# Kernel tuning notes

Measured on AMD Instinct MI355X. Metric: run time of the kernel, lower is better.

The kernel has to match this reference:

```python
import jax, jax.numpy as jnp
import numpy as np

B, T, DIM, H, HD = 2, 2048, 1024, 16, 64
ROPE_THETA = 500000.0
EPS = 1e-6
SOFTCAP = 50.0


def _rmsnorm(x, gamma):
    # x: (..., HD)
    rms = jax.lax.rsqrt(jnp.mean(x * x, axis=-1, keepdims=True) + EPS)
    return x * rms * gamma


def _apply_rope(x, cos, sin):
    # x: (B, T, H, HD); cos/sin: (T, HD//2). Pairs are interleaved (even, odd).
    xe = x[..., 0::2]
    xo = x[..., 1::2]
    c = cos[None, :, None, :]
    s = sin[None, :, None, :]
    re = xe * c - xo * s
    im = xe * s + xo * c
    # re-interleave: (..., HD//2, 2) -> (..., HD)
    return jnp.stack([re, im], axis=-1).reshape(x.shape)


def setup_inputs() -> dict:
    key = jax.random.key(0)
    kx, kq, kk, kv, ko = jax.random.split(key, 5)
    x = jax.random.normal(kx, (B, T, DIM), dtype=jnp.float32)
    sc = 0.02
    wq = jax.random.normal(kq, (H * HD, DIM), dtype=jnp.float32) * sc
    wk = jax.random.normal(kk, (HD, DIM), dtype=jnp.float32) * sc
    wv = jax.random.normal(kv, (HD, DIM), dtype=jnp.float32) * sc
    wo = jax.random.normal(ko, (DIM, H * HD), dtype=jnp.float32) * sc
    q_gamma = jnp.ones((HD,), dtype=jnp.float32)
    k_gamma = jnp.ones((HD,), dtype=jnp.float32)
    # RoPE tables (same as torch.polar precompute)
    inv_freq = 1.0 / (ROPE_THETA ** (np.arange(0, HD, 2, dtype=np.float32) / HD))
    t = np.arange(T, dtype=np.float32)
    ang = np.outer(t, inv_freq)  # (T, HD//2)
    freqs_cos = jnp.asarray(np.cos(ang), dtype=jnp.float32)
    freqs_sin = jnp.asarray(np.sin(ang), dtype=jnp.float32)
    # causal additive mask (T, T)
    causal = np.tril(np.ones((T, T), dtype=bool))
    mask = jnp.asarray(np.where(causal, 0.0, -1e9).astype(np.float32))
    return {"x": x, "wq": wq, "wk": wk, "wv": wv, "wo": wo,
            "q_gamma": q_gamma, "k_gamma": k_gamma,
            "freqs_cos": freqs_cos, "freqs_sin": freqs_sin, "mask": mask}


def reference(x, wq, wk, wv, wo, q_gamma, k_gamma, freqs_cos, freqs_sin, mask):
    b, t, _ = x.shape
    q = (x @ wq.T).reshape(b, t, H, HD)            # (B,T,H,HD)
    k = (x @ wk.T).reshape(b, t, 1, HD)            # (B,T,1,HD) single KV head
    v = x @ wv.T                                    # (B,T,HD)
    q = _rmsnorm(q, q_gamma)
    k = _rmsnorm(k, k_gamma)
    q = _apply_rope(q, freqs_cos, freqs_sin)
    k = _apply_rope(k, freqs_cos, freqs_sin)[:, :, 0, :]  # (B,S,HD)
    scale = HD ** -0.5
    # MQA: single K/V head shared across H query heads
    attn = jnp.einsum('bthd,bsd->bhts', q, k) * scale      # (B,H,T,S)
    attn = jnp.tanh(attn / SOFTCAP) * SOFTCAP
    attn = attn + mask[None, None, :, :]
    p = jax.nn.softmax(attn, axis=-1)
    out = jnp.einsum('bhts,bsd->bthd', p, v).reshape(b, t, H * HD)
    return out @ wo.T
```

## Files before the change

kernel.cpp:

```cpp
#include <hip/hip_runtime.h>
#include <hip/hip_bf16.h>
#include <stdint.h>
#include <math.h>

#define B_ 2
#define T_ 2048
#define DIM_ 1024
#define H_ 16
#define HD_ 64
#define NROWS_ (B_*T_)
#define NQKV 1152
#define UNITS_PER_BH 80
#define NUNITS (16 * UNITS_PER_BH)

typedef __bf16 bf16_t;
typedef __attribute__((ext_vector_type(8))) __bf16 bf16x8;
typedef __attribute__((ext_vector_type(4))) __bf16 bf16x4;
typedef __attribute__((ext_vector_type(4))) float f32x4;
typedef __attribute__((ext_vector_type(16))) float f32x16;

__device__ __forceinline__ float wave_sum64(float v) {
#pragma unroll
  for (int off = 32; off > 0; off >>= 1) v += __shfl_xor(v, off, 64);
  return v;
}

__device__ __forceinline__ int cb(int q) {
  int a = q >> 3, r = q & 7;
  return 4 * a * (a + 1) + r * (a + 1);
}

__device__ __forceinline__ bf16_t* swz(bf16_t* base, int row, int col) {
  return (bf16_t*)((char*)base + (row << 7) + (((col << 1) ^ ((row & 7) << 4))));
}

__device__ __forceinline__ f32x16 mfma32(bf16x8 a, bf16x8 b, f32x16 c) {
  return __builtin_amdgcn_mfma_f32_32x32x16_bf16(a, b, c, 0, 0, 0);
}

__device__ __forceinline__ unsigned cvt_pk(float lo, float hi) {
  unsigned r;
  asm("v_cvt_pk_bf16_f32 %0, %1, %2" : "=v"(r) : "v"(lo), "v"(hi));
  return r;
}
__device__ __forceinline__ void plswap(unsigned& x, unsigned& y) {
  asm volatile("v_permlane32_swap_b32 %0, %1" : "+v"(x), "+v"(y));
}

#define C_S0 (NROWS_*DIM_/8)
#define C_S1 (C_S0 + DIM_*DIM_/8)
#define C_S2 (C_S1 + HD_*DIM_/8)
#define C_S3 (C_S2 + HD_*DIM_/8)
#define C_S4 (C_S3 + DIM_*DIM_/8)
__global__ __launch_bounds__(256) void cvt_all(
    const float* __restrict__ x, const float* __restrict__ wq,
    const float* __restrict__ wk, const float* __restrict__ wv,
    const float* __restrict__ wo, bf16_t* __restrict__ xb,
    bf16_t* __restrict__ wqkvb, bf16_t* __restrict__ wob) {
  int i = blockIdx.x * 256 + threadIdx.x;
  if (i >= C_S4) return;
  const float* src; bf16_t* dst; int j;
  if (i < C_S0)      { src = x;  dst = xb; j = i; }
  else if (i < C_S1) { src = wq; dst = wqkvb; j = i - C_S0; }
  else if (i < C_S2) { src = wk; dst = wqkvb + (size_t)DIM_ * DIM_; j = i - C_S1; }
  else if (i < C_S3) { src = wv; dst = wqkvb + (size_t)(DIM_ + HD_) * DIM_; j = i - C_S2; }
  else               { src = wo; dst = wob; j = i - C_S3; }
  float4 a = ((const float4*)src)[2 * (size_t)j];
  float4 b = ((const float4*)src)[2 * (size_t)j + 1];
  bf16x8 o;
  o[0] = (bf16_t)a.x; o[1] = (bf16_t)a.y; o[2] = (bf16_t)a.z; o[3] = (bf16_t)a.w;
  o[4] = (bf16_t)b.x; o[5] = (bf16_t)b.y; o[6] = (bf16_t)b.z; o[7] = (bf16_t)b.w;
  *(bf16x8*)(dst + 8 * (size_t)j) = o;
}

template<int OUTF32, int QKV>
__global__ __launch_bounds__(256) void gemm_bt(const bf16_t* __restrict__ A,
    const bf16_t* __restrict__ Bw, void* __restrict__ Cv,
    bf16_t* __restrict__ vt, int N, int K) {
  __shared__ bf16_t As[128 * 32];
  __shared__ bf16_t Bs[64 * 32];
  const int tid = threadIdx.x;
  const int w = tid >> 6, lane = tid & 63;
  const int row0 = blockIdx.x * 128, col0 = blockIdx.y * 64;
  const int wm = w >> 1, wn = w & 1;
  const int rr = lane & 15, kg = lane >> 4;
  f32x4 acc[4][2];
#pragma unroll
  for (int i = 0; i < 4; ++i)
#pragma unroll
    for (int j = 0; j < 2; ++j) acc[i][j] = (f32x4){0.f, 0.f, 0.f, 0.f};
  const int srow = lane >> 2;
  const int skoff = ((lane & 3) ^ (srow & 3)) << 3;
  for (int kt = 0; kt < K; kt += 32) {
    __syncthreads();
#pragma unroll
    for (int c = 0; c < 2; ++c) {
      const int chunk = 2 * w + c;
      const bf16_t* sA = A + (size_t)(row0 + chunk * 16 + srow) * K + kt + skoff;
      __builtin_amdgcn_global_load_lds(
          (const __attribute__((address_space(1))) unsigned int*)(uintptr_t)sA,
          (__attribute__((address_space(3))) unsigned int*)(uintptr_t)(As + chunk * 512),
          16, 0, 0);
    }
    {
      const bf16_t* sB = Bw + (size_t)(col0 + w * 16 + srow) * K + kt + skoff;
      __builtin_amdgcn_global_load_lds(
          (const __attribute__((address_space(1))) unsigned int*)(uintptr_t)sB,
          (__attribute__((address_space(3))) unsigned int*)(uintptr_t)(Bs + w * 512),
          16, 0, 0);
    }
    __syncthreads();
    bf16x8 af[4], bfv[2];
#pragma unroll
    for (int mi = 0; mi < 4; ++mi) {
      int r = 64 * wm + 16 * mi + rr;
      af[mi] = *(const bf16x8*)(As + r * 32 + ((kg ^ (r & 3)) << 3));
    }
#pragma unroll
    for (int ni = 0; ni < 2; ++ni) {
      int r = 32 * wn + 16 * ni + rr;
      bfv[ni] = *(const bf16x8*)(Bs + r * 32 + ((kg ^ (r & 3)) << 3));
    }
#pragma unroll
    for (int mi = 0; mi < 4; ++mi)
#pragma unroll
      for (int ni = 0; ni < 2; ++ni)
        acc[mi][ni] = __builtin_amdgcn_mfma_f32_16x16x32_bf16(af[mi], bfv[ni],
                                                              acc[mi][ni], 0, 0, 0);
  }
  const int crow = (lane >> 4) * 4, ccol = lane & 15;
  if (QKV && col0 == DIM_ + HD_) {
#pragma unroll
    for (int mi = 0; mi < 4; ++mi)
#pragma unroll
      for (int ni = 0; ni < 2; ++ni) {
        int d = 32 * wn + 16 * ni + ccol;
        size_t rg = (size_t)(row0 + 64 * wm + 16 * mi + crow);
        bf16x4 pk;
#pragma unroll
        for (int r = 0; r < 4; ++r) pk[r] = (bf16_t)acc[mi][ni][r];
        *(bf16x4*)(vt + (size_t)d * NROWS_ + rg) = pk;
      }
  } else {
#pragma unroll
    for (int mi = 0; mi < 4; ++mi)
#pragma unroll
      for (int ni = 0; ni < 2; ++ni)
#pragma unroll
        for (int r = 0; r < 4; ++r) {
          size_t rg = (size_t)(row0 + 64 * wm + 16 * mi + crow + r);
          size_t cg = (size_t)(col0 + 32 * wn + 16 * ni + ccol);
          if (OUTF32) ((float*)Cv)[rg * N + cg] = acc[mi][ni][r];
          else        ((bf16_t*)Cv)[rg * N + cg] = (bf16_t)acc[mi][ni][r];
        }
  }
}

__global__ __launch_bounds__(512) void normrope(bf16_t* __restrict__ qkv,
    const float* __restrict__ qg, const float* __restrict__ kgm,
    const float* __restrict__ fc, const float* __restrict__ fs) {
  const int row = blockIdx.x;
  const int w = threadIdx.x >> 6, d = threadIdx.x & 63;
  const int t = row & (T_ - 1);
  const float c = fc[t * (HD_ / 2) + (d >> 1)];
  const float s = fs[t * (HD_ / 2) + (d >> 1)];
  for (int hh = w; hh <= H_; hh += 8) {
    bf16_t* ptr = qkv + (size_t)row * NQKV + hh * HD_;
    float g = (hh < H_) ? qg[d] : kgm[d];
    float val = (float)ptr[d];
    float ssum = wave_sum64(val * val);
    float rms = rsqrtf(ssum * (1.f / HD_) + 1e-6f);
    val *= rms * g;
    float partner = __shfl_xor(val, 1, 64);
    float res = ((d & 1) == 0) ? (val * c - partner * s) : (partner * s + val * c);
    ptr[d] = (bf16_t)res;
  }
}

__global__ __launch_bounds__(512, 4) void attn_part(const bf16_t* __restrict__ qkv,
                                                    const bf16_t* __restrict__ vt,
                                                    bf16_t* __restrict__ partO,
                                                    float* __restrict__ partL) {
  __shared__ __align__(16) char SMEM[32768];
  __shared__ float Lx[4][32];
  bf16_t* Ks = (bf16_t*)SMEM;
  bf16_t* Vt = (bf16_t*)(SMEM + 16384);
  const int tid = threadIdx.x;
  const int w = tid >> 6, lane = tid & 63;
  const int u = blockIdx.x;
  const int bh = u / UNITS_PER_BH;
  const int rem = u - bh * UNITS_PER_BH;
  const int b = bh >> 3, hp = bh & 7;
  int qt = 0;
  while (qt < 31 && cb(qt + 1) <= rem) ++qt;
  const int chunk = rem - cb(qt);
  const int nt = min(8, qt + 1 - chunk * 8);
  const int NP = (nt + 1) >> 1;
  const int qt0 = qt * 64;
  const int h0 = hp * 2;
  const size_t bT = (size_t)b * T_;
  const int lo = lane & 31, hi = lane >> 5;
  const int hw = w >> 2, qg = (w >> 1) & 1, ks = w & 1, g2 = w >> 1;

  bf16x8 qf[4];
  {
    const bf16_t* qbase =
        qkv + (bT + qt0 + 32 * qg + lo) * NQKV + (h0 + hw) * HD_ + hi * 8;
#pragma unroll
    for (int s = 0; s < 4; ++s) qf[s] = *(const bf16x8*)(qbase + 16 * s);
  }
  const int srow = tid >> 3, scol = (tid & 7) * 8;
  const bf16_t* kp = qkv + (bT + chunk * 512 + srow) * NQKV + DIM_ + scol;
  const bf16_t* vtp = vt + (size_t)srow * NROWS_ + bT + chunk * 512 + scol;
  uint4 kpre0, kpre1, vpre0, vpre1;

#define PREFETCH() do {                                                       \
    kpre0 = *(const uint4*)kp;                                                \
    kpre1 = *(const uint4*)(kp + (size_t)64 * NQKV);                          \
    vpre0 = *(const uint4*)vtp;                                               \
    vpre1 = *(const uint4*)(vtp + 64);                                        \
    kp += (size_t)128 * NQKV;                                                 \
    vtp += 128;                                                               \
  } while (0)
#define STAGE() do {                                                          \
    *(uint4*)swz(Ks, srow, scol) = kpre0;                                     \
    *(uint4*)swz(Ks + 4096, srow, scol) = kpre1;                              \
    *(uint4*)swz(Vt, srow, scol) = vpre0;                                     \
    *(uint4*)swz(Vt + 4096, srow, scol) = vpre1;                              \
  } while (0)

  f32x16 accO0 = {}, accO1 = {};
  float l_ = 0.f;
  bf16_t* KsP = Ks + ks * 4096;
  bf16_t* VtP = Vt + ks * 4096;

  PREFETCH();
  STAGE();
  if (NP > 1) PREFETCH();
  __syncthreads();

  for (int j = 0; j < NP; ++j) {
    const int ctl = 2 * j + ks;
    if (ctl < nt) {
      const int ct = chunk * 8 + ctl;
      f32x16 S0 = {}, S1 = {};
      __builtin_amdgcn_s_setprio(1);
#pragma unroll
      for (int s = 0; s < 4; ++s) {
        bf16x8 kf0 = *(const bf16x8*)swz(KsP, lo, 16 * s + hi * 8);
        bf16x8 kf1 = *(const bf16x8*)swz(KsP, 32 + lo, 16 * s + hi * 8);
        S0 = mfma32(kf0, qf[s], S0);
        S1 = mfma32(kf1, qf[s], S1);
      }
      __builtin_amdgcn_s_setprio(0);
      const bool full = (64 * ct + 63 <= qt0 + 32 * qg);
      const int qrel = qt0 + 32 * qg + lo - 64 * ct;
      float psum = 0.f;
#pragma unroll
      for (int kh = 0; kh < 2; ++kh)
#pragma unroll
        for (int r = 0; r < 16; ++r) {
          float sv = (kh == 0) ? S0[r] : S1[r];
          float u2 = sv * sv * 6.25e-6f;
          float poly = fmaf(u2, 0.13333334f, -0.33333334f);
          float poly2 = fmaf(u2, poly, 1.0f);
          float pv = __expf(fmaf(sv * 0.125f, poly2, -16.f));
          if (!full) {
            int koff = 32 * kh + (r & 3) + 8 * (r >> 2) + 4 * hi;
            pv = (koff <= qrel) ? pv : 0.f;
          }
          psum += pv;
          if (kh == 0) S0[r] = pv; else S1[r] = pv;
        }
      psum += __shfl_xor(psum, 32, 64);
      l_ += psum;
      __builtin_amdgcn_s_setprio(1);
#pragma unroll
      for (int s = 0; s < 4; ++s) {
        const int base = (s & 1) * 8;
        float p0, p1, p2, p3, p4, p5, p6, p7;
        if (s >> 1) {
          p0 = S1[base + 0]; p1 = S1[base + 1]; p2 = S1[base + 2]; p3 = S1[base + 3];
          p4 = S1[base + 4]; p5 = S1[base + 5]; p6 = S1[base + 6]; p7 = S1[base + 7];
        } else {
          p0 = S0[base + 0]; p1 = S0[base + 1]; p2 = S0[base + 2]; p3 = S0[base + 3];
          p4 = S0[base + 4]; p5 = S0[base + 5]; p6 = S0[base + 6]; p7 = S0[base + 7];
        }
        unsigned a0 = cvt_pk(p0, p1), a1 = cvt_pk(p2, p3);
        unsigned b0 = cvt_pk(p4, p5), b1 = cvt_pk(p6, p7);
        plswap(a0, b0);
        plswap(a1, b1);
        union { unsigned uu[4]; bf16x8 v; } pa;
        pa.uu[0] = a0; pa.uu[1] = a1; pa.uu[2] = b0; pa.uu[3] = b1;
        bf16x8 vf0 = *(const bf16x8*)swz(VtP, lo, 16 * s + hi * 8);
        bf16x8 vf1 = *(const bf16x8*)swz(VtP, 32 + lo, 16 * s + hi * 8);
        accO0 = mfma32(pa.v, vf0, accO0);
        accO1 = mfma32(pa.v, vf1, accO1);
      }
      __builtin_amdgcn_s_setprio(0);
    }
    __syncthreads();
    if (j + 1 < NP) {
      STAGE();
      if (j + 2 < NP) PREFETCH();
      __syncthreads();
    }
  }
#undef PREFETCH
#undef STAGE

  float* exch = (float*)SMEM;
  float* my = exch + ((size_t)g2 * 64 + lane) * 32;
  if (ks == 1) {
#pragma unroll
    for (int qd = 0; qd < 4; ++qd) {
      int sl = (qd ^ (lane & 7)) * 4;
      f32x4 t0 = {accO0[4*qd], accO0[4*qd+1], accO0[4*qd+2], accO0[4*qd+3]};
      *(f32x4*)(my + sl) = t0;
      int sl2 = ((qd + 4) ^ (lane & 7)) * 4;
      f32x4 t1 = {accO1[4*qd], accO1[4*qd+1], accO1[4*qd+2], accO1[4*qd+3]};
      *(f32x4*)(my + sl2) = t1;
    }
    if (hi == 0) Lx[g2][lo] = l_;
  }
  __syncthreads();
  if (ks == 0) {
#pragma unroll
    for (int qd = 0; qd < 4; ++qd) {
      int sl = (qd ^ (lane & 7)) * 4;
      f32x4 t0 = *(const f32x4*)(my + sl);
      accO0[4*qd] += t0[0]; accO0[4*qd+1] += t0[1];
      accO0[4*qd+2] += t0[2]; accO0[4*qd+3] += t0[3];
      int sl2 = ((qd + 4) ^ (lane & 7)) * 4;
      f32x4 t1 = *(const f32x4*)(my + sl2);
      accO1[4*qd] += t1[0]; accO1[4*qd+1] += t1[1];
      accO1[4*qd+2] += t1[2]; accO1[4*qd+3] += t1[3];
    }
    float l_tot = l_ + Lx[g2][lo];
    bf16_t* po = partO + ((size_t)u * 2 + hw) * 4096;
#pragma unroll
    for (int rq = 0; rq < 4; ++rq)
#pragma unroll
      for (int c = 0; c < 4; ++c) {
        int q = 32 * qg + 8 * rq + 4 * hi + c;
        po[q * 64 + lo] = (bf16_t)accO0[4 * rq + c];
        po[q * 64 + 32 + lo] = (bf16_t)accO1[4 * rq + c];
      }
    if (hi == 0) partL[((size_t)u * 2 + hw) * 64 + 32 * qg + lo] = l_tot;
  }
}

__global__ __launch_bounds__(256) void attn_reduce(const bf16_t* __restrict__ partO,
                                                   const float* __restrict__ partL,
                                                   bf16_t* __restrict__ att) {
  const int qt = blockIdx.x, h = blockIdx.y, b = blockIdx.z;
  const int nch = (qt + 8) >> 3;
  const size_t ubase = (size_t)(b * 8 + (h >> 1)) * UNITS_PER_BH + cb(qt);
  const int hw = h & 1;
  const int tid = threadIdx.x;
  const int q = tid >> 2, dblk = (tid & 3) * 16;
  f32x4 o[4] = {};
  float l = 0.f;
  for (int c = 0; c < nch; ++c) {
    const bf16_t* po = partO + ((ubase + c) * 2 + hw) * 4096 + q * 64 + dblk;
    bf16x8 v0 = *(const bf16x8*)po;
    bf16x8 v1 = *(const bf16x8*)(po + 8);
#pragma unroll
    for (int i = 0; i < 4; ++i) o[0][i] += (float)v0[i];
#pragma unroll
    for (int i = 0; i < 4; ++i) o[1][i] += (float)v0[4 + i];
#pragma unroll
    for (int i = 0; i < 4; ++i) o[2][i] += (float)v1[i];
#pragma unroll
    for (int i = 0; i < 4; ++i) o[3][i] += (float)v1[4 + i];
    l += partL[((ubase + c) * 2 + hw) * 64 + q];
  }
  const float linv = 1.f / l;
  bf16_t* dst = att + ((size_t)(b * T_ + qt * 64 + q)) * DIM_ + h * HD_ + dblk;
  bf16x8 r0, r1;
#pragma unroll
  for (int i = 0; i < 4; ++i) { r0[i] = (bf16_t)(o[0][i] * linv);
                                r0[4+i] = (bf16_t)(o[1][i] * linv);
                                r1[i] = (bf16_t)(o[2][i] * linv);
                                r1[4+i] = (bf16_t)(o[3][i] * linv); }
  *(bf16x8*)dst = r0;
  *(bf16x8*)(dst + 8) = r1;
}

extern "C" void kernel_launch(void* const* d_in, const int* in_sizes, int n_in,
                              void* d_out, int out_size, void* d_ws, size_t ws_size,
                              hipStream_t stream) {
  const float* x   = (const float*)d_in[0];
  const float* wq  = (const float*)d_in[1];
  const float* wk  = (const float*)d_in[2];
  const float* wv  = (const float*)d_in[3];
  const float* wo  = (const float*)d_in[4];
  const float* qg  = (const float*)d_in[5];
  const float* kgm = (const float*)d_in[6];
  const float* fc  = (const float*)d_in[7];
  const float* fs  = (const float*)d_in[8];
  float* out = (float*)d_out;

  bf16_t* xb    = (bf16_t*)d_ws;
  bf16_t* wqkvb = xb + (size_t)NROWS_ * DIM_;
  bf16_t* wob   = wqkvb + (size_t)NQKV * DIM_;
  bf16_t* qkvo  = wob + (size_t)DIM_ * DIM_;
  bf16_t* attb  = qkvo + (size_t)NROWS_ * NQKV;
  bf16_t* partO = attb + (size_t)NROWS_ * DIM_;
  float*  partL = (float*)(partO + (size_t)NUNITS * 2 * 4096);
  bf16_t* vtb   = (bf16_t*)(partL + (size_t)NUNITS * 2 * 64);

  cvt_all<<<(C_S4 + 255) / 256, 256, 0, stream>>>(x, wq, wk, wv, wo, xb, wqkvb, wob);
  gemm_bt<0, 1><<<dim3(NROWS_ / 128, NQKV / 64), 256, 0, stream>>>(
      xb, wqkvb, qkvo, vtb, NQKV, DIM_);
  normrope<<<NROWS_, 512, 0, stream>>>(qkvo, qg, kgm, fc, fs);
  attn_part<<<NUNITS, 512, 0, stream>>>(qkvo, vtb, partO, partL);
  attn_reduce<<<dim3(T_ / 64, H_, B_), 256, 0, stream>>>(partO, partL, attb);
  gemm_bt<1, 0><<<dim3(NROWS_ / 128, DIM_ / 64), 256, 0, stream>>>(
      attb, wob, out, nullptr, DIM_, DIM_);
}
```

Baseline: 119.9 us.

## Fold softcap scale into Q, reschedule attention blocks, double K-step GEMM

Several changes at once. The tanh-softcap polynomial is re-expressed in base-2 with the scale folded into the normalized Q at normrope time, and the masked and full branches are split. The row sum now uses dot2 bf16 on the packed probabilities, and attention work units are issued in reverse order so the heaviest causal blocks start first. The QKV/output GEMM also loads two 32-wide K slices per sync, halving the barriers. Summing the bf16-rounded probabilities makes the normalizer match the values fed to the PV MFMA, but it changes the numerics slightly.

```diff
diff --git a/kernel.cpp b/kernel.cpp
--- a/kernel.cpp
+++ b/kernel.cpp
@@ -12,6 +12,9 @@
 #define NQKV 1152
 #define UNITS_PER_BH 80
 #define NUNITS (16 * UNITS_PER_BH)
+#define CT_SCALE 0.18033688f
+#define C2_ (-6.40603e-5f)
+#define C4_ (4.92447e-9f)
 
 typedef __bf16 bf16_t;
 typedef __attribute__((ext_vector_type(8))) __bf16 bf16x8;
@@ -45,6 +48,11 @@
 }
 __device__ __forceinline__ void plswap(unsigned& x, unsigned& y) {
   asm volatile("v_permlane32_swap_b32 %0, %1" : "+v"(x), "+v"(y));
+}
+__device__ __forceinline__ float dot2bf(unsigned a, unsigned b, float c) {
+  float d;
+  asm("v_dot2_f32_bf16 %0, %1, %2, %3" : "=v"(d) : "v"(a), "v"(b), "v"(c));
+  return d;
 }
 
 #define C_S0 (NROWS_*DIM_/8)
@@ -77,8 +85,8 @@
 __global__ __launch_bounds__(256) void gemm_bt(const bf16_t* __restrict__ A,
     const bf16_t* __restrict__ Bw, void* __restrict__ Cv,
     bf16_t* __restrict__ vt, int N, int K) {
-  __shared__ bf16_t As[128 * 32];
-  __shared__ bf16_t Bs[64 * 32];
+  __shared__ bf16_t As[2][128 * 32];
+  __shared__ bf16_t Bs[2][64 * 32];
   const int tid = threadIdx.x;
   const int w = tid >> 6, lane = tid & 63;
   const int row0 = blockIdx.x * 128, col0 = blockIdx.y * 64;
@@ -91,42 +99,48 @@
     for (int j = 0; j < 2; ++j) acc[i][j] = (f32x4){0.f, 0.f, 0.f, 0.f};
   const int srow = lane >> 2;
   const int skoff = ((lane & 3) ^ (srow & 3)) << 3;
-  for (int kt = 0; kt < K; kt += 32) {
+  for (int kt = 0; kt < K; kt += 64) {
     __syncthreads();
 #pragma unroll
-    for (int c = 0; c < 2; ++c) {
-      const int chunk = 2 * w + c;
-      const bf16_t* sA = A + (size_t)(row0 + chunk * 16 + srow) * K + kt + skoff;
-      __builtin_amdgcn_global_load_lds(
-          (const __attribute__((address_space(1))) unsigned int*)(uintptr_t)sA,
-          (__attribute__((address_space(3))) unsigned int*)(uintptr_t)(As + chunk * 512),
-          16, 0, 0);
-    }
-    {
-      const bf16_t* sB = Bw + (size_t)(col0 + w * 16 + srow) * K + kt + skoff;
+    for (int kk = 0; kk < 2; ++kk) {
+#pragma unroll
+      for (int c = 0; c < 2; ++c) {
+        const int chunk = 2 * w + c;
+        const bf16_t* sA =
+            A + (size_t)(row0 + chunk * 16 + srow) * K + kt + 32 * kk + skoff;
+        __builtin_amdgcn_global_load_lds(
+            (const __attribute__((address_space(1))) unsigned int*)(uintptr_t)sA,
+            (__attribute__((address_space(3))) unsigned int*)(uintptr_t)(&As[kk][chunk * 512]),
+            16, 0, 0);
+      }
+      const bf16_t* sB =
+          Bw + (size_t)(col0 + w * 16 + srow) * K + kt + 32 * kk + skoff;
       __builtin_amdgcn_global_load_lds(
           (const __attribute__((address_space(1))) unsigned int*)(uintptr_t)sB,
-          (__attribute__((address_space(3))) unsigned int*)(uintptr_t)(Bs + w * 512),
+          (__attribute__((address_space(3))) unsigned int*)(uintptr_t)(&Bs[kk][w * 512]),
           16, 0, 0);
     }
     __syncthreads();
-    bf16x8 af[4], bfv[2];
-#pragma unroll
-    for (int mi = 0; mi < 4; ++mi) {
-      int r = 64 * wm + 16 * mi + rr;
-      af[mi] = *(const bf16x8*)(As + r * 32 + ((kg ^ (r & 3)) << 3));
-    }
-#pragma unroll
-    for (int ni = 0; ni < 2; ++ni) {
-      int r = 32 * wn + 16 * ni + rr;
-      bfv[ni] = *(const bf16x8*)(Bs + r * 32 + ((kg ^ (r & 3)) << 3));
-    }
-#pragma unroll
-    for (int mi = 0; mi < 4; ++mi)
-#pragma unroll
-      for (int ni = 0; ni < 2; ++ni)
-        acc[mi][ni] = __builtin_amdgcn_mfma_f32_16x16x32_bf16(af[mi], bfv[ni],
-                                                              acc[mi][ni], 0, 0, 0);
+#pragma unroll
+    for (int kk = 0; kk < 2; ++kk) {
+      bf16x8 af[4], bfv[2];
+#pragma unroll
+      for (int mi = 0; mi < 4; ++mi) {
+        int r = 64 * wm + 16 * mi + rr;
+        af[mi] = *(const bf16x8*)(&As[kk][r * 32 + ((kg ^ (r & 3)) << 3)]);
+      }
+#pragma unroll
+      for (int ni = 0; ni < 2; ++ni) {
+        int r = 32 * wn + 16 * ni + rr;
+        bfv[ni] = *(const bf16x8*)(&Bs[kk][r * 32 + ((kg ^ (r & 3)) << 3)]);
+      }
+#pragma unroll
+      for (int mi = 0; mi < 4; ++mi)
+#pragma unroll
+        for (int ni = 0; ni < 2; ++ni)
+          acc[mi][ni] = __builtin_amdgcn_mfma_f32_16x16x32_bf16(af[mi], bfv[ni],
+                                                                acc[mi][ni], 0, 0, 0);
+    }
   }
   const int crow = (lane >> 4) * 4, ccol = lane & 15;
   if (QKV && col0 == DIM_ + HD_) {
@@ -173,6 +187,7 @@
     val *= rms * g;
     float partner = __shfl_xor(val, 1, 64);
     float res = ((d & 1) == 0) ? (val * c - partner * s) : (partner * s + val * c);
+    if (hh < H_) res *= CT_SCALE;
     ptr[d] = (bf16_t)res;
   }
 }
@@ -187,7 +202,7 @@
   bf16_t* Vt = (bf16_t*)(SMEM + 16384);
   const int tid = threadIdx.x;
   const int w = tid >> 6, lane = tid & 63;
-  const int u = blockIdx.x;
+  const int u = NUNITS - 1 - (int)blockIdx.x;
   const int bh = u / UNITS_PER_BH;
   const int rem = u - bh * UNITS_PER_BH;
   const int b = bh >> 3, hp = bh & 7;
@@ -231,6 +246,7 @@
 
   f32x16 accO0 = {}, accO1 = {};
   float l_ = 0.f;
+  const unsigned ones2 = 0x3F803F80u;
   bf16_t* KsP = Ks + ks * 4096;
   bf16_t* VtP = Vt + ks * 4096;
 
@@ -254,26 +270,35 @@
       }
       __builtin_amdgcn_s_setprio(0);
       const bool full = (64 * ct + 63 <= qt0 + 32 * qg);
-      const int qrel = qt0 + 32 * qg + lo - 64 * ct;
-      float psum = 0.f;
-#pragma unroll
-      for (int kh = 0; kh < 2; ++kh)
-#pragma unroll
-        for (int r = 0; r < 16; ++r) {
-          float sv = (kh == 0) ? S0[r] : S1[r];
-          float u2 = sv * sv * 6.25e-6f;
-          float poly = fmaf(u2, 0.13333334f, -0.33333334f);
-          float poly2 = fmaf(u2, poly, 1.0f);
-          float pv = __expf(fmaf(sv * 0.125f, poly2, -16.f));
-          if (!full) {
+      if (full) {
+#pragma unroll
+        for (int kh = 0; kh < 2; ++kh)
+#pragma unroll
+          for (int r = 0; r < 16; ++r) {
+            float t = (kh == 0) ? S0[r] : S1[r];
+            float t2 = t * t;
+            float ww = fmaf(t2, C4_, C2_);
+            float t3 = t * t2;
+            float pv = exp2f(fmaf(t3, ww, t));
+            if (kh == 0) S0[r] = pv; else S1[r] = pv;
+          }
+      } else {
+        const int qrel = qt0 + 32 * qg + lo - 64 * ct;
+#pragma unroll
+        for (int kh = 0; kh < 2; ++kh)
+#pragma unroll
+          for (int r = 0; r < 16; ++r) {
+            float t = (kh == 0) ? S0[r] : S1[r];
+            float t2 = t * t;
+            float ww = fmaf(t2, C4_, C2_);
+            float t3 = t * t2;
+            float pv = exp2f(fmaf(t3, ww, t));
             int koff = 32 * kh + (r & 3) + 8 * (r >> 2) + 4 * hi;
             pv = (koff <= qrel) ? pv : 0.f;
+            if (kh == 0) S0[r] = pv; else S1[r] = pv;
           }
-          psum += pv;
-          if (kh == 0) S0[r] = pv; else S1[r] = pv;
-        }
-      psum += __shfl_xor(psum, 32, 64);
-      l_ += psum;
+      }
+      float psA = 0.f, psB = 0.f;
       __builtin_amdgcn_s_setprio(1);
 #pragma unroll
       for (int s = 0; s < 4; ++s) {
@@ -290,6 +315,10 @@
         unsigned b0 = cvt_pk(p4, p5), b1 = cvt_pk(p6, p7);
         plswap(a0, b0);
         plswap(a1, b1);
+        psA = dot2bf(a0, ones2, psA);
+        psB = dot2bf(a1, ones2, psB);
+        psA = dot2bf(b0, ones2, psA);
+        psB = dot2bf(b1, ones2, psB);
         union { unsigned uu[4]; bf16x8 v; } pa;
         pa.uu[0] = a0; pa.uu[1] = a1; pa.uu[2] = b0; pa.uu[3] = b1;
         bf16x8 vf0 = *(const bf16x8*)swz(VtP, lo, 16 * s + hi * 8);
@@ -298,6 +327,9 @@
         accO1 = mfma32(pa.v, vf1, accO1);
       }
       __builtin_amdgcn_s_setprio(0);
+      float psum = psA + psB;
+      psum += __shfl_xor(psum, 32, 64);
+      l_ += psum;
     }
     __syncthreads();
     if (j + 1 < NP) {
```

Measured after the change: 147.5 us. 23.1% more time.
